# Kernel tuning notes

Hardware: AMD Instinct MI355X
Metric: run time of the kernel (lower is better)

## Reference

```python
import jax, jax.numpy as jnp
import numpy as np
import math

B, LQ, LK = 4, 1024, 2048
QD, KD, VD = 768, 512, 512
H, NH = 1024, 16
HD = H // NH

def setup_inputs() -> dict:
    key = jax.random.key(0)
    ks = jax.random.split(key, 11)
    s = 0.02
    return {
        "query": jax.random.normal(ks[0], (B, LQ, QD), jnp.float32),
        "key": jax.random.normal(ks[1], (B, LK, KD), jnp.float32),
        "value": jax.random.normal(ks[2], (B, LK, VD), jnp.float32),
        "Wq": jax.random.normal(ks[3], (QD, H), jnp.float32) * s,
        "bq": jnp.zeros((H,), jnp.float32),
        "Wk": jax.random.normal(ks[4], (KD, H), jnp.float32) * s,
        "bk": jnp.zeros((H,), jnp.float32),
        "Wv": jax.random.normal(ks[5], (VD, H), jnp.float32) * s,
        "bv": jnp.zeros((H,), jnp.float32),
        "Wo": jax.random.normal(ks[6], (H, H), jnp.float32) * s,
        "bo": jnp.zeros((H,), jnp.float32),
    }

def reference(query, key, value, Wq, bq, Wk, bk, Wv, bv, Wo, bo):
    # project and split heads: [B, L, H] -> [B, NH, L, HD]
    def heads(x):
        b, l, _ = x.shape
        return x.reshape(b, l, NH, HD).transpose(0, 2, 1, 3)
    q = heads(query @ Wq + bq)   # [B, NH, LQ, HD]
    k = heads(key @ Wk + bk)     # [B, NH, LK, HD]
    v = heads(value @ Wv + bv)   # [B, NH, LK, HD]
    scores = jnp.einsum('bhqd,bhkd->bhqk', q, k) / math.sqrt(HD)
    weights = jax.nn.softmax(scores, axis=-1)  # dropout inactive (eval / rate used deterministically as identity)
    att = jnp.einsum('bhqk,bhkd->bhqd', weights, v)
    att = att.transpose(0, 2, 1, 3).reshape(query.shape[0], -1, H)
    out = att @ Wo + bo
    return out
```

## Files before the change

kernel.cpp:

```cpp
#include <hip/hip_runtime.h>
#include <math.h>

using bf16x8 = __attribute__((ext_vector_type(8))) short;
using f32x4  = __attribute__((ext_vector_type(4))) float;

namespace {
constexpr int kB  = 4;
constexpr int kLQ = 1024;
constexpr int kLK = 2048;
constexpr int kH  = 1024;
constexpr int kHD = 64;
}

__device__ __forceinline__ unsigned short f2bf(float x) {
  union { float f; unsigned int u; } v; v.f = x;
  unsigned int r = v.u + 0x7fffu + ((v.u >> 16) & 1u);
  return (unsigned short)(r >> 16);
}

typedef const __attribute__((address_space(1))) unsigned int guint_t;
typedef __attribute__((address_space(3))) unsigned int luint_t;
__device__ __forceinline__ void g2l16(const void* g, void* l) {
  __builtin_amdgcn_global_load_lds(
      (guint_t*)g,
      (luint_t*)(unsigned int)(unsigned long long)l,
      16, 0, 0);
}

__global__ __launch_bounds__(256) void prep_kernel(
    const float* __restrict__ q, const float* __restrict__ k,
    const float* __restrict__ v, const float* __restrict__ Wq,
    const float* __restrict__ Wk, const float* __restrict__ Wv,
    const float* __restrict__ Wo, unsigned short* __restrict__ qo,
    unsigned short* __restrict__ ko, unsigned short* __restrict__ vo,
    unsigned short* __restrict__ WqT, unsigned short* __restrict__ WkT,
    unsigned short* __restrict__ WvT, unsigned short* __restrict__ WoT)
{
  __shared__ float tile[64][65];
  const int t = threadIdx.x;
  if (blockIdx.x < 5632) {
    int c = blockIdx.x * 256 + t;
    const float* src; unsigned short* dst;
    if (c < 393216)      { src = q; dst = qo; }
    else if (c < 917504) { src = k; dst = ko; c -= 393216; }
    else                 { src = v; dst = vo; c -= 917504; }
    const int i = c * 8;
    const float4 a = *(const float4*)(src + i);
    const float4 b = *(const float4*)(src + i + 4);
    uint4 o;
    o.x = (unsigned int)f2bf(a.x) | ((unsigned int)f2bf(a.y) << 16);
    o.y = (unsigned int)f2bf(a.z) | ((unsigned int)f2bf(a.w) << 16);
    o.z = (unsigned int)f2bf(b.x) | ((unsigned int)f2bf(b.y) << 16);
    o.w = (unsigned int)f2bf(b.z) | ((unsigned int)f2bf(b.w) << 16);
    *(uint4*)(dst + i) = o;
    return;
  }
  int id = blockIdx.x - 5632;
  const float* W; unsigned short* Wt; int Kd;
  if (id < 192)      { W = Wq; Wt = WqT; Kd = 768; }
  else if (id < 320) { W = Wk; Wt = WkT; Kd = 512;  id -= 192; }
  else if (id < 448) { W = Wv; Wt = WvT; Kd = 512;  id -= 320; }
  else               { W = Wo; Wt = WoT; Kd = 1024; id -= 448; }
  const int Nd = 1024;
  const int n0 = (id & 15) * 64;
  const int k0 = (id >> 4) * 64;
  const int rr = t >> 4;
  const int c4 = t & 15;
#pragma unroll
  for (int i = 0; i < 4; ++i) {
    const int row = i * 16 + rr;
    const float4 vv = *(const float4*)(W + (size_t)(k0 + row) * Nd + n0 + c4 * 4);
    tile[row][c4*4+0] = vv.x; tile[row][c4*4+1] = vv.y;
    tile[row][c4*4+2] = vv.z; tile[row][c4*4+3] = vv.w;
  }
  __syncthreads();
#pragma unroll
  for (int i = 0; i < 4; ++i) {
    const int n = i * 16 + rr;
    ushort4 o;
    o.x = f2bf(tile[c4*4+0][n]); o.y = f2bf(tile[c4*4+1][n]);
    o.z = f2bf(tile[c4*4+2][n]); o.w = f2bf(tile[c4*4+3][n]);
    *(ushort4*)(Wt + (size_t)(n0 + n) * Kd + k0 + c4 * 4) = o;
  }
}

__device__ __forceinline__ void gemm_body256(
    const unsigned short* __restrict__ A, const unsigned short* __restrict__ Bt,
    const float* __restrict__ bias, unsigned short* __restrict__ Cout,
    int N, int K, int bx, int by, int mode, char* lds)
{
  const int t    = threadIdx.x;
  const int lane = t & 63;
  const int w    = t >> 6;
  const int l15  = lane & 15;
  const int lq8  = (lane >> 4) * 8;
  const int lq4  = (lane >> 4) * 4;
  const int r0   = by * 128;
  const int c0   = bx * 256;
  const int wm   = w >> 1, wn = w & 1;

  f32x4 acc[4][8] = {};

#pragma unroll
  for (int i = 0; i < 6; ++i) {
    const int g = w * 6 + i;
    const unsigned short* src = (g < 8) ? A : Bt;
    const int rbase = (g < 8) ? (r0 + g * 16) : (c0 + (g - 8) * 16);
    g2l16(src + (size_t)(rbase + l15) * K + lq8, lds + g * 1024 + lane * 16);
  }

  int pb = 0;
  for (int k0 = 0; k0 < K; k0 += 32, pb ^= 1) {
    __syncthreads();
    char* buf = lds + pb * 24576;
    if (k0 + 32 < K) {
      char* nbuf = lds + (pb ^ 1) * 24576;
#pragma unroll
      for (int i = 0; i < 6; ++i) {
        const int g = w * 6 + i;
        const unsigned short* src = (g < 8) ? A : Bt;
        const int rbase = (g < 8) ? (r0 + g * 16) : (c0 + (g - 8) * 16);
        g2l16(src + (size_t)(rbase + l15) * K + k0 + 32 + lq8, nbuf + g * 1024 + lane * 16);
      }
    }
    bf16x8 af[4], bfr[8];
#pragma unroll
    for (int i = 0; i < 4; ++i) af[i]  = *(const bf16x8*)(buf + (wm*4 + i) * 1024 + lane * 16);
#pragma unroll
    for (int j = 0; j < 8; ++j) bfr[j] = *(const bf16x8*)(buf + 8192 + (wn*8 + j) * 1024 + lane * 16);
#pragma unroll
    for (int i = 0; i < 4; ++i)
#pragma unroll
      for (int j = 0; j < 8; ++j)
        acc[i][j] = __builtin_amdgcn_mfma_f32_16x16x32_bf16(af[i], bfr[j], acc[i][j], 0, 0, 0);
  }

#pragma unroll
  for (int j = 0; j < 8; ++j) {
    const int col = c0 + wn * 128 + j * 16 + l15;
    const float bcol = bias[col];
#pragma unroll
    for (int i = 0; i < 4; ++i) {
      const int row = r0 + wm * 64 + i * 16 + lq4;
      if (mode == 1) {
#pragma unroll
        for (int r = 0; r < 4; ++r) Cout[(size_t)(row + r) * N + col] = f2bf(acc[i][j][r] + bcol);
      } else {
        const int bb = row >> 11;
        const int lk = row & 2047;
        ushort4 o;
        o.x = f2bf(acc[i][j][0] + bcol); o.y = f2bf(acc[i][j][1] + bcol);
        o.z = f2bf(acc[i][j][2] + bcol); o.w = f2bf(acc[i][j][3] + bcol);
        *(ushort4*)(Cout + (size_t)(bb * kH + col) * kLK + lk) = o;
      }
    }
  }
}

__global__ __launch_bounds__(256) void qkv_gemm_kernel(
    const unsigned short* __restrict__ qA, const unsigned short* __restrict__ WqT,
    const float* __restrict__ bq, unsigned short* __restrict__ Qb,
    const unsigned short* __restrict__ kA, const unsigned short* __restrict__ WkT,
    const float* __restrict__ bk, unsigned short* __restrict__ Kb,
    const unsigned short* __restrict__ vA, const unsigned short* __restrict__ WvT,
    const float* __restrict__ bv, unsigned short* __restrict__ Vtw)
{
  __shared__ __align__(16) char lds[49152];
  int id = blockIdx.x;
  if (id < 128) {
    gemm_body256(qA, WqT, bq, Qb, 1024, 768, id & 3, id >> 2, 1, lds);
  } else if (id < 384) {
    id -= 128;
    gemm_body256(kA, WkT, bk, Kb, 1024, 512, id & 3, id >> 2, 1, lds);
  } else {
    id -= 384;
    gemm_body256(vA, WvT, bv, Vtw, 1024, 512, id & 3, id >> 2, 2, lds);
  }
}

__global__ __launch_bounds__(256) void out_gemm_kernel(
    const unsigned short* __restrict__ A, const unsigned short* __restrict__ Bt,
    const float* __restrict__ bias, float* __restrict__ C)
{
  __shared__ __align__(16) char lds[32768];
  const int t    = threadIdx.x;
  const int lane = t & 63;
  const int w    = t >> 6;
  const int l15  = lane & 15;
  const int lq8  = (lane >> 4) * 8;
  const int lq4  = (lane >> 4) * 4;
  const int r0   = blockIdx.y * 128;
  const int c0   = blockIdx.x * 128;
  const int wm   = w >> 1, wn = w & 1;
  const int N = 1024, K = 1024;

  f32x4 acc[4][4] = {};

#pragma unroll
  for (int i = 0; i < 4; ++i) {
    const int g = w * 4 + i;
    const unsigned short* src = (g < 8) ? A : Bt;
    const int rbase = (g < 8) ? (r0 + g * 16) : (c0 + (g - 8) * 16);
    g2l16(src + (size_t)(rbase + l15) * K + lq8, lds + g * 1024 + lane * 16);
  }
  int pb = 0;
  for (int k0 = 0; k0 < K; k0 += 32, pb ^= 1) {
    __syncthreads();
    char* buf = lds + pb * 16384;
    if (k0 + 32 < K) {
      char* nbuf = lds + (pb ^ 1) * 16384;
#pragma unroll
      for (int i = 0; i < 4; ++i) {
        const int g = w * 4 + i;
        const unsigned short* src = (g < 8) ? A : Bt;
        const int rbase = (g < 8) ? (r0 + g * 16) : (c0 + (g - 8) * 16);
        g2l16(src + (size_t)(rbase + l15) * K + k0 + 32 + lq8, nbuf + g * 1024 + lane * 16);
      }
    }
    bf16x8 af[4], bfr[4];
#pragma unroll
    for (int i = 0; i < 4; ++i) af[i]  = *(const bf16x8*)(buf + (wm*4 + i) * 1024 + lane * 16);
#pragma unroll
    for (int j = 0; j < 4; ++j) bfr[j] = *(const bf16x8*)(buf + 8192 + (wn*4 + j) * 1024 + lane * 16);
#pragma unroll
    for (int i = 0; i < 4; ++i)
#pragma unroll
      for (int j = 0; j < 4; ++j)
        acc[i][j] = __builtin_amdgcn_mfma_f32_16x16x32_bf16(af[i], bfr[j], acc[i][j], 0, 0, 0);
  }
#pragma unroll
  for (int j = 0; j < 4; ++j) {
    const int col = c0 + wn * 64 + j * 16 + l15;
    const float bcol = bias[col];
#pragma unroll
    for (int i = 0; i < 4; ++i) {
      const int row = r0 + wm * 64 + i * 16 + lq4;
#pragma unroll
      for (int r = 0; r < 4; ++r) C[(size_t)(row + r) * N + col] = acc[i][j][r] + bcol;
    }
  }
}

__global__ __launch_bounds__(256) void attn_mfma_kernel(
    const unsigned short* __restrict__ Q, const unsigned short* __restrict__ K,
    const unsigned short* __restrict__ Vt, unsigned short* __restrict__ O)
{
  __shared__ __align__(16) char lds[61440];
  constexpr int VOFF = 16384;
  constexpr int POFF = 24576;
  const int t    = threadIdx.x;
  const int lane = t & 63;
  const int w    = t >> 6;
  const int l15  = lane & 15;
  const int lq8  = (lane >> 4) * 8;
  const int lq4  = (lane >> 4) * 4;
  const int flat = blockIdx.x;
  const int bh   = flat & 63;
  const int qb   = flat >> 6;
  const int h    = bh & 15;
  const int b    = bh >> 4;
  const int q0   = qb * 256;
  const int hoff = h * kHD;
  const int qw   = w * 64;

  bf16x8 qf[4][2];
#pragma unroll
  for (int qi = 0; qi < 4; ++qi)
#pragma unroll
    for (int kh = 0; kh < 2; ++kh)
      qf[qi][kh] = *(const bf16x8*)(Q + (size_t)(b*kLQ + q0 + qw + qi*16 + l15) * kH
                                      + hoff + kh*32 + lq8);

  f32x4 acc[4][4] = {};
  float lsum[4][4] = {};

#pragma unroll
  for (int i = 0; i < 2; ++i) {
    const int g = w * 2 + i;
    g2l16(K + (size_t)(b*kLK + (g >> 1)*16 + l15) * kH + hoff + (g & 1)*32 + lq8,
          lds + g * 1024 + lane * 16);
  }

  for (int kt = 0; kt < kLK / 64; ++kt) {
    const int kc0 = kt * 64;
    char* kbuf = lds + (kt & 1) * 8192;
    __syncthreads();

#pragma unroll
    for (int i = 0; i < 2; ++i) {
      const int gg = w * 2 + i;
      g2l16(Vt + (size_t)(b*kH + hoff + (gg >> 1)*16 + l15) * kLK + kc0 + (gg & 1)*32 + lq8,
            lds + VOFF + gg * 1024 + lane * 16);
    }
    if (kt + 1 < kLK / 64) {
      const int kc1 = kc0 + 64;
      char* nkbuf = lds + ((kt + 1) & 1) * 8192;
#pragma unroll
      for (int i = 0; i < 2; ++i) {
        const int g = w * 2 + i;
        g2l16(K + (size_t)(b*kLK + kc1 + (g >> 1)*16 + l15) * kH + hoff + (g & 1)*32 + lq8,
              nkbuf + g * 1024 + lane * 16);
      }
    }

    f32x4 s[4][4];
#pragma unroll
    for (int kcf = 0; kcf < 4; ++kcf) {
      const bf16x8 kf0 = *(const bf16x8*)(kbuf + (kcf*2 + 0) * 1024 + lane * 16);
      const bf16x8 kf1 = *(const bf16x8*)(kbuf + (kcf*2 + 1) * 1024 + lane * 16);
#pragma unroll
      for (int qi = 0; qi < 4; ++qi) {
        f32x4 z = {};
        z = __builtin_amdgcn_mfma_f32_16x16x32_bf16(qf[qi][0], kf0, z, 0, 0, 0);
        z = __builtin_amdgcn_mfma_f32_16x16x32_bf16(qf[qi][1], kf1, z, 0, 0, 0);
        s[qi][kcf] = z;
      }
    }

#pragma unroll
    for (int qi = 0; qi < 4; ++qi)
#pragma unroll
      for (int kcf = 0; kcf < 4; ++kcf)
#pragma unroll
        for (int r = 0; r < 4; ++r) {
          const float p = __builtin_amdgcn_exp2f(s[qi][kcf][r] * 0.18033688011112042f);
          lsum[qi][r] += p;
          union { float f; unsigned int u; } pu; pu.f = p;
          *(unsigned short*)(lds + POFF +
              ((qw + qi*16 + lq4 + r) * 72 + kcf*16 + l15) * 2) =
              (unsigned short)(pu.u >> 16);
        }

    __syncthreads();

    bf16x8 pf[4][2];
#pragma unroll
    for (int qi = 0; qi < 4; ++qi)
#pragma unroll
      for (int kq = 0; kq < 2; ++kq)
        pf[qi][kq] = *(const bf16x8*)(lds + POFF +
            ((qw + qi*16 + l15) * 72 + kq*32 + lq8) * 2);
#pragma unroll
    for (int vd = 0; vd < 4; ++vd) {
      const bf16x8 vf0 = *(const bf16x8*)(lds + VOFF + (vd*2 + 0) * 1024 + lane * 16);
      const bf16x8 vf1 = *(const bf16x8*)(lds + VOFF + (vd*2 + 1) * 1024 + lane * 16);
#pragma unroll
      for (int qi = 0; qi < 4; ++qi) {
        acc[qi][vd] = __builtin_amdgcn_mfma_f32_16x16x32_bf16(pf[qi][0], vf0, acc[qi][vd], 0, 0, 0);
        acc[qi][vd] = __builtin_amdgcn_mfma_f32_16x16x32_bf16(pf[qi][1], vf1, acc[qi][vd], 0, 0, 0);
      }
    }
  }

#pragma unroll
  for (int qi = 0; qi < 4; ++qi)
#pragma unroll
    for (int r = 0; r < 4; ++r) {
      float v = lsum[qi][r];
      v += __shfl_xor(v, 1);
      v += __shfl_xor(v, 2);
      v += __shfl_xor(v, 4);
      v += __shfl_xor(v, 8);
      lsum[qi][r] = 1.f / v;
    }
#pragma unroll
  for (int qi = 0; qi < 4; ++qi)
#pragma unroll
    for (int vd = 0; vd < 4; ++vd)
#pragma unroll
      for (int r = 0; r < 4; ++r)
        O[(size_t)(b*kLQ + q0 + qw + qi*16 + lq4 + r) * kH + hoff + vd*16 + l15] =
            f2bf(acc[qi][vd][r] * lsum[qi][r]);
}

extern "C" void kernel_launch(void* const* d_in, const int* in_sizes, int n_in,
                              void* d_out, int out_size, void* d_ws, size_t ws_size,
                              hipStream_t stream) {
  (void)in_sizes; (void)n_in; (void)out_size; (void)ws_size;
  const float* query = (const float*)d_in[0];
  const float* key   = (const float*)d_in[1];
  const float* value = (const float*)d_in[2];
  const float* Wq = (const float*)d_in[3];
  const float* bq = (const float*)d_in[4];
  const float* Wk = (const float*)d_in[5];
  const float* bk = (const float*)d_in[6];
  const float* Wv = (const float*)d_in[7];
  const float* bv = (const float*)d_in[8];
  const float* Wo = (const float*)d_in[9];
  const float* bo = (const float*)d_in[10];
  float* out = (float*)d_out;

  unsigned short* ws  = (unsigned short*)d_ws;
  unsigned short* qA  = ws;
  unsigned short* kA  = qA  + 3145728;
  unsigned short* vA  = kA  + 4194304;
  unsigned short* WqT = vA  + 4194304;
  unsigned short* WkT = WqT + 786432;
  unsigned short* WvT = WkT + 524288;
  unsigned short* WoT = WvT + 524288;
  unsigned short* Qb  = WoT + 1048576;
  unsigned short* Kb  = Qb  + 4194304;
  unsigned short* Vtw = Kb  + 8388608;
  unsigned short* Ab  = Vtw + 8388608;

  dim3 blk(256);
  prep_kernel<<<6336, blk, 0, stream>>>(query, key, value, Wq, Wk, Wv, Wo,
                                        qA, kA, vA, WqT, WkT, WvT, WoT);
  qkv_gemm_kernel<<<640, blk, 0, stream>>>(qA, WqT, bq, Qb,
                                           kA, WkT, bk, Kb,
                                           vA, WvT, bv, Vtw);
  attn_mfma_kernel<<<256, blk, 0, stream>>>(Qb, Kb, Vtw, Ab);
  out_gemm_kernel<<<dim3(8, 32), blk, 0, stream>>>(Ab, WoT, bo, out);
}
```

Measured before the change: 260.8 us.

## Split attention over key halves with 32x32 MFMA and a reduce pass

The attention kernel now splits the key dimension into two halves, launching twice as many blocks. Each block writes unnormalized fp32 partial outputs and row sums, and a new reduce kernel combines them and normalizes into bf16. The inner loops also move from 16x16x32 to 32x32x16 MFMA tiles, prefetch both K and V tiles into double-buffered LDS, and keep the P tile per-wave, which removes one barrier per iteration. This raises occupancy across the GPU's CUs but adds fp32 partial-result traffic and an extra kernel launch.

```diff
diff --git a/kernel.cpp b/kernel.cpp
--- a/kernel.cpp
+++ b/kernel.cpp
@@ -3,6 +3,7 @@
 
 using bf16x8 = __attribute__((ext_vector_type(8))) short;
 using f32x4  = __attribute__((ext_vector_type(4))) float;
+using f32x16 = __attribute__((ext_vector_type(16))) float;
 
 namespace {
 constexpr int kB  = 4;
@@ -16,6 +17,10 @@
   union { float f; unsigned int u; } v; v.f = x;
   unsigned int r = v.u + 0x7fffu + ((v.u >> 16) & 1u);
   return (unsigned short)(r >> 16);
+}
+__device__ __forceinline__ unsigned int bfT(float x) {
+  union { float f; unsigned int u; } v; v.f = x;
+  return v.u >> 16;
 }
 
 typedef const __attribute__((address_space(1))) unsigned int guint_t;
@@ -243,134 +248,162 @@
 
 __global__ __launch_bounds__(256) void attn_mfma_kernel(
     const unsigned short* __restrict__ Q, const unsigned short* __restrict__ K,
-    const unsigned short* __restrict__ Vt, unsigned short* __restrict__ O)
-{
-  __shared__ __align__(16) char lds[61440];
-  constexpr int VOFF = 16384;
-  constexpr int POFF = 24576;
+    const unsigned short* __restrict__ Vt, float* __restrict__ Op0,
+    float* __restrict__ Op1, float* __restrict__ Ls)
+{
+  __shared__ __align__(16) char lds[65536];
   const int t    = threadIdx.x;
   const int lane = t & 63;
   const int w    = t >> 6;
-  const int l15  = lane & 15;
-  const int lq8  = (lane >> 4) * 8;
-  const int lq4  = (lane >> 4) * 4;
+  const int l31  = lane & 31;
+  const int h    = lane >> 5;
   const int flat = blockIdx.x;
   const int bh   = flat & 63;
-  const int qb   = flat >> 6;
-  const int h    = bh & 15;
+  const int g8   = flat >> 6;
+  const int s    = g8 & 1;
+  const int qb   = g8 >> 1;
+  const int hh   = bh & 15;
   const int b    = bh >> 4;
   const int q0   = qb * 256;
-  const int hoff = h * kHD;
-  const int qw   = w * 64;
-
-  bf16x8 qf[4][2];
-#pragma unroll
-  for (int qi = 0; qi < 4; ++qi)
-#pragma unroll
-    for (int kh = 0; kh < 2; ++kh)
-      qf[qi][kh] = *(const bf16x8*)(Q + (size_t)(b*kLQ + q0 + qw + qi*16 + l15) * kH
-                                      + hoff + kh*32 + lq8);
-
-  f32x4 acc[4][4] = {};
-  float lsum[4][4] = {};
-
-#pragma unroll
-  for (int i = 0; i < 2; ++i) {
-    const int g = w * 2 + i;
-    g2l16(K + (size_t)(b*kLK + (g >> 1)*16 + l15) * kH + hoff + (g & 1)*32 + lq8,
-          lds + g * 1024 + lane * 16);
-  }
-
-  for (int kt = 0; kt < kLK / 64; ++kt) {
-    const int kc0 = kt * 64;
+  const int kcb  = s * 1024;
+  const int hoff = hh * kHD;
+  const int qw   = q0 + w * 64;
+
+  bf16x8 qf[2][4];
+#pragma unroll
+  for (int qt2 = 0; qt2 < 2; ++qt2)
+#pragma unroll
+    for (int ds_ = 0; ds_ < 4; ++ds_)
+      qf[qt2][ds_] = *(const bf16x8*)(Q + (size_t)(b*kLQ + qw + qt2*32 + l31) * kH
+                                        + hoff + ds_*16 + h*8);
+
+  f32x16 oacc[2][2] = {};
+  float lsum[2] = {0.f, 0.f};
+
+#pragma unroll
+  for (int i = 0; i < 4; ++i) {
+    const int g = w * 4 + i;
+    if (g < 8) {
+      g2l16(K + (size_t)(b*kLK + kcb + (g >> 2)*32 + l31) * kH + hoff + (g & 3)*16 + h*8,
+            lds + g * 1024 + lane * 16);
+    } else {
+      const int gg = g - 8;
+      g2l16(Vt + (size_t)(b*kH + hoff + (gg >> 2)*32 + l31) * kLK + kcb + (gg & 3)*16 + h*8,
+            lds + 16384 + gg * 1024 + lane * 16);
+    }
+  }
+
+  char* const pbase = lds + 32768 + w * 8192;
+
+  for (int kt = 0; kt < 16; ++kt) {
+    __syncthreads();
     char* kbuf = lds + (kt & 1) * 8192;
-    __syncthreads();
-
-#pragma unroll
-    for (int i = 0; i < 2; ++i) {
-      const int gg = w * 2 + i;
-      g2l16(Vt + (size_t)(b*kH + hoff + (gg >> 1)*16 + l15) * kLK + kc0 + (gg & 1)*32 + lq8,
-            lds + VOFF + gg * 1024 + lane * 16);
-    }
-    if (kt + 1 < kLK / 64) {
-      const int kc1 = kc0 + 64;
-      char* nkbuf = lds + ((kt + 1) & 1) * 8192;
-#pragma unroll
-      for (int i = 0; i < 2; ++i) {
-        const int g = w * 2 + i;
-        g2l16(K + (size_t)(b*kLK + kc1 + (g >> 1)*16 + l15) * kH + hoff + (g & 1)*32 + lq8,
-              nkbuf + g * 1024 + lane * 16);
-      }
-    }
-
-    f32x4 s[4][4];
-#pragma unroll
-    for (int kcf = 0; kcf < 4; ++kcf) {
-      const bf16x8 kf0 = *(const bf16x8*)(kbuf + (kcf*2 + 0) * 1024 + lane * 16);
-      const bf16x8 kf1 = *(const bf16x8*)(kbuf + (kcf*2 + 1) * 1024 + lane * 16);
-#pragma unroll
-      for (int qi = 0; qi < 4; ++qi) {
-        f32x4 z = {};
-        z = __builtin_amdgcn_mfma_f32_16x16x32_bf16(qf[qi][0], kf0, z, 0, 0, 0);
-        z = __builtin_amdgcn_mfma_f32_16x16x32_bf16(qf[qi][1], kf1, z, 0, 0, 0);
-        s[qi][kcf] = z;
-      }
-    }
-
-#pragma unroll
-    for (int qi = 0; qi < 4; ++qi)
-#pragma unroll
-      for (int kcf = 0; kcf < 4; ++kcf)
-#pragma unroll
-        for (int r = 0; r < 4; ++r) {
-          const float p = __builtin_amdgcn_exp2f(s[qi][kcf][r] * 0.18033688011112042f);
-          lsum[qi][r] += p;
-          union { float f; unsigned int u; } pu; pu.f = p;
-          *(unsigned short*)(lds + POFF +
-              ((qw + qi*16 + lq4 + r) * 72 + kcf*16 + l15) * 2) =
-              (unsigned short)(pu.u >> 16);
+    char* vbuf = lds + 16384 + (kt & 1) * 8192;
+    if (kt + 1 < 16) {
+      char* nk = lds + ((kt + 1) & 1) * 8192;
+      char* nv = lds + 16384 + ((kt + 1) & 1) * 8192;
+      const int kc1 = kcb + (kt + 1) * 64;
+#pragma unroll
+      for (int i = 0; i < 4; ++i) {
+        const int g = w * 4 + i;
+        if (g < 8) {
+          g2l16(K + (size_t)(b*kLK + kc1 + (g >> 2)*32 + l31) * kH + hoff + (g & 3)*16 + h*8,
+                nk + g * 1024 + lane * 16);
+        } else {
+          const int gg = g - 8;
+          g2l16(Vt + (size_t)(b*kH + hoff + (gg >> 2)*32 + l31) * kLK + kc1 + (gg & 3)*16 + h*8,
+                nv + gg * 1024 + lane * 16);
         }
-
-    __syncthreads();
-
-    bf16x8 pf[4][2];
-#pragma unroll
-    for (int qi = 0; qi < 4; ++qi)
-#pragma unroll
-      for (int kq = 0; kq < 2; ++kq)
-        pf[qi][kq] = *(const bf16x8*)(lds + POFF +
-            ((qw + qi*16 + l15) * 72 + kq*32 + lq8) * 2);
-#pragma unroll
-    for (int vd = 0; vd < 4; ++vd) {
-      const bf16x8 vf0 = *(const bf16x8*)(lds + VOFF + (vd*2 + 0) * 1024 + lane * 16);
-      const bf16x8 vf1 = *(const bf16x8*)(lds + VOFF + (vd*2 + 1) * 1024 + lane * 16);
-#pragma unroll
-      for (int qi = 0; qi < 4; ++qi) {
-        acc[qi][vd] = __builtin_amdgcn_mfma_f32_16x16x32_bf16(pf[qi][0], vf0, acc[qi][vd], 0, 0, 0);
-        acc[qi][vd] = __builtin_amdgcn_mfma_f32_16x16x32_bf16(pf[qi][1], vf1, acc[qi][vd], 0, 0, 0);
-      }
-    }
-  }
-
-#pragma unroll
-  for (int qi = 0; qi < 4; ++qi)
-#pragma unroll
-    for (int r = 0; r < 4; ++r) {
-      float v = lsum[qi][r];
-      v += __shfl_xor(v, 1);
-      v += __shfl_xor(v, 2);
-      v += __shfl_xor(v, 4);
-      v += __shfl_xor(v, 8);
-      lsum[qi][r] = 1.f / v;
-    }
-#pragma unroll
-  for (int qi = 0; qi < 4; ++qi)
-#pragma unroll
-    for (int vd = 0; vd < 4; ++vd)
-#pragma unroll
-      for (int r = 0; r < 4; ++r)
-        O[(size_t)(b*kLQ + q0 + qw + qi*16 + lq4 + r) * kH + hoff + vd*16 + l15] =
-            f2bf(acc[qi][vd][r] * lsum[qi][r]);
+      }
+    }
+
+    f32x16 sacc[2][2] = {};
+#pragma unroll
+    for (int ds_ = 0; ds_ < 4; ++ds_) {
+      const bf16x8 kf0 = *(const bf16x8*)(kbuf + (0*4 + ds_) * 1024 + lane * 16);
+      const bf16x8 kf1 = *(const bf16x8*)(kbuf + (1*4 + ds_) * 1024 + lane * 16);
+#pragma unroll
+      for (int qt2 = 0; qt2 < 2; ++qt2) {
+        sacc[0][qt2] = __builtin_amdgcn_mfma_f32_32x32x16_bf16(kf0, qf[qt2][ds_], sacc[0][qt2], 0, 0, 0);
+        sacc[1][qt2] = __builtin_amdgcn_mfma_f32_32x32x16_bf16(kf1, qf[qt2][ds_], sacc[1][qt2], 0, 0, 0);
+      }
+    }
+
+#pragma unroll
+    for (int kct2 = 0; kct2 < 2; ++kct2)
+#pragma unroll
+      for (int qt2 = 0; qt2 < 2; ++qt2)
+#pragma unroll
+        for (int g4 = 0; g4 < 4; ++g4) {
+          const float e0 = __builtin_amdgcn_exp2f(sacc[kct2][qt2][g4*4+0] * 0.18033688011112042f);
+          const float e1 = __builtin_amdgcn_exp2f(sacc[kct2][qt2][g4*4+1] * 0.18033688011112042f);
+          const float e2 = __builtin_amdgcn_exp2f(sacc[kct2][qt2][g4*4+2] * 0.18033688011112042f);
+          const float e3 = __builtin_amdgcn_exp2f(sacc[kct2][qt2][g4*4+3] * 0.18033688011112042f);
+          lsum[qt2] += (e0 + e1) + (e2 + e3);
+          uint2 u;
+          u.x = bfT(e0) | (bfT(e1) << 16);
+          u.y = bfT(e2) | (bfT(e3) << 16);
+          *(uint2*)(pbase + (qt2*4 + kct2*2 + (g4 >> 1)) * 1024 +
+                    (((g4 & 1) * 32) + l31) * 16 + 8*h) = u;
+        }
+
+#pragma unroll
+    for (int ks = 0; ks < 4; ++ks) {
+      const bf16x8 pf0 = *(const bf16x8*)(pbase + (0*4 + ks) * 1024 + lane * 16);
+      const bf16x8 pf1 = *(const bf16x8*)(pbase + (1*4 + ks) * 1024 + lane * 16);
+      const bf16x8 vf0 = *(const bf16x8*)(vbuf + (0*4 + ks) * 1024 + lane * 16);
+      const bf16x8 vf1 = *(const bf16x8*)(vbuf + (1*4 + ks) * 1024 + lane * 16);
+      oacc[0][0] = __builtin_amdgcn_mfma_f32_32x32x16_bf16(pf0, vf0, oacc[0][0], 0, 0, 0);
+      oacc[0][1] = __builtin_amdgcn_mfma_f32_32x32x16_bf16(pf0, vf1, oacc[0][1], 0, 0, 0);
+      oacc[1][0] = __builtin_amdgcn_mfma_f32_32x32x16_bf16(pf1, vf0, oacc[1][0], 0, 0, 0);
+      oacc[1][1] = __builtin_amdgcn_mfma_f32_32x32x16_bf16(pf1, vf1, oacc[1][1], 0, 0, 0);
+    }
+  }
+
+#pragma unroll
+  for (int qt2 = 0; qt2 < 2; ++qt2)
+    lsum[qt2] += __shfl_xor(lsum[qt2], 32);
+
+  float* Op = s ? Op1 : Op0;
+#pragma unroll
+  for (int qt2 = 0; qt2 < 2; ++qt2)
+#pragma unroll
+    for (int dt = 0; dt < 2; ++dt)
+#pragma unroll
+      for (int r = 0; r < 16; ++r) {
+        const int qrow = qw + qt2*32 + (r & 3) + 8*(r >> 2) + 4*h;
+        Op[(size_t)bh * 65536 + (size_t)qrow * 64 + dt*32 + l31] = oacc[qt2][dt][r];
+      }
+  if (h == 0) {
+#pragma unroll
+    for (int qt2 = 0; qt2 < 2; ++qt2)
+      Ls[(size_t)s * 65536 + bh * 1024 + qw + qt2*32 + l31] = lsum[qt2];
+  }
+}
+
+__global__ __launch_bounds__(256) void attn_reduce_kernel(
+    const float* __restrict__ Op0, const float* __restrict__ Op1,
+    const float* __restrict__ Ls, unsigned short* __restrict__ Ab)
+{
+  const int g   = blockIdx.x * 256 + threadIdx.x;
+  const int bhq = g >> 3;
+  const int d8  = (g & 7) * 8;
+  const float inv = 1.f / (Ls[bhq] + Ls[65536 + bhq]);
+  const size_t base = (size_t)bhq * 64 + d8;
+  const float4 a0 = *(const float4*)(Op0 + base);
+  const float4 a1 = *(const float4*)(Op0 + base + 4);
+  const float4 b0 = *(const float4*)(Op1 + base);
+  const float4 b1 = *(const float4*)(Op1 + base + 4);
+  const int bh = bhq >> 10, qq = bhq & 1023;
+  const int bb = bh >> 4, hh = bh & 15;
+  unsigned short* dst = Ab + (size_t)(bb * kLQ + qq) * kH + hh * 64 + d8;
+  ushort4 o0, o1;
+  o0.x = f2bf((a0.x + b0.x) * inv); o0.y = f2bf((a0.y + b0.y) * inv);
+  o0.z = f2bf((a0.z + b0.z) * inv); o0.w = f2bf((a0.w + b0.w) * inv);
+  o1.x = f2bf((a1.x + b1.x) * inv); o1.y = f2bf((a1.y + b1.y) * inv);
+  o1.z = f2bf((a1.z + b1.z) * inv); o1.w = f2bf((a1.w + b1.w) * inv);
+  *(ushort4*)dst = o0;
+  *(ushort4*)(dst + 4) = o1;
 }
 
 extern "C" void kernel_launch(void* const* d_in, const int* in_sizes, int n_in,
@@ -403,12 +436,17 @@
   unsigned short* Vtw = Kb  + 8388608;
   unsigned short* Ab  = Vtw + 8388608;
 
+  float* Op0 = (float*)ws;
+  float* Lsp = Op0 + 4194304;
+  float* Op1 = (float*)(Ab + 4194304);
+
   dim3 blk(256);
   prep_kernel<<<6336, blk, 0, stream>>>(query, key, value, Wq, Wk, Wv, Wo,
                                         qA, kA, vA, WqT, WkT, WvT, WoT);
   qkv_gemm_kernel<<<640, blk, 0, stream>>>(qA, WqT, bq, Qb,
                                            kA, WkT, bk, Kb,
                                            vA, WvT, bv, Vtw);
-  attn_mfma_kernel<<<256, blk, 0, stream>>>(Qb, Kb, Vtw, Ab);
+  attn_mfma_kernel<<<512, blk, 0, stream>>>(Qb, Kb, Vtw, Op0, Op1, Lsp);
+  attn_reduce_kernel<<<2048, blk, 0, stream>>>(Op0, Op1, Lsp, Ab);
   out_gemm_kernel<<<dim3(8, 32), blk, 0, stream>>>(Ab, WoT, bo, out);
 }
```

New measurement: 265.4 us. About the same (+1.7%).
